# Kernel tuning notes

Hardware: AMD Instinct MI355X
Metric: run time of the kernel (lower is better)

## Reference

```python
import jax, jax.numpy as jnp
import numpy as np

D_MODEL = 1024
H = 16
D_K = D_MODEL // H
B = 128   # batch (intersample attention attends across this dim)
N = 256   # samples / tokens per row


def setup_inputs() -> dict:
    key = jax.random.key(0)
    ks = jax.random.split(key, 8)
    s = 1.0 / np.sqrt(D_MODEL)
    return {
        "query": jax.random.normal(ks[0], (B, N, D_MODEL), jnp.float32),
        "key":   jax.random.normal(ks[1], (B, N, D_MODEL), jnp.float32),
        "value": jax.random.normal(ks[2], (B, N, D_MODEL), jnp.float32),
        "Wq": jax.random.normal(ks[3], (D_MODEL, D_MODEL), jnp.float32) * s,
        "bq": jnp.zeros((D_MODEL,), jnp.float32),
        "Wk": jax.random.normal(ks[4], (D_MODEL, D_MODEL), jnp.float32) * s,
        "bk": jnp.zeros((D_MODEL,), jnp.float32),
        "Wv": jax.random.normal(ks[5], (D_MODEL, D_MODEL), jnp.float32) * s,
        "bv": jnp.zeros((D_MODEL,), jnp.float32),
        "Wo": jax.random.normal(ks[6], (D_MODEL, D_MODEL), jnp.float32) * s,
        "bo": jnp.zeros((D_MODEL,), jnp.float32),
    }


def _proj_heads(x, W, b):
    # torch nn.Linear: x @ W.T + b ; then view (b, n, h, d_k) -> (b, h, n, d_k)
    y = jnp.einsum('bnd,ed->bne', x, W) + b
    bsz, n, _ = y.shape
    return y.reshape(bsz, n, H, D_K).transpose(0, 2, 1, 3)


def reference(query, key, value, Wq, bq, Wk, bk, Wv, bv, Wo, bo):
    q = _proj_heads(query, Wq, bq)  # (b, h, n, d_k)
    k = _proj_heads(key,   Wk, bk)
    v = _proj_heads(value, Wv, bv)
    # intersample attention: attend ACROSS the batch dim b (per head, per sample n)
    scale = 1.0 / jnp.sqrt(jnp.asarray(D_K, q.dtype))
    scores = jnp.einsum('bhnd,chnd->hnbc', q, k) * scale  # (h, n, b, b)
    p = jax.nn.softmax(scores, axis=-1)
    out = jnp.einsum('hnbc,chnd->bhnd', p, v)             # (b, h, n, d_k)
    # merge heads: (b, h, n, d_k) -> (b, n, h*d_k)
    bsz, _, n, _ = out.shape
    out = out.transpose(0, 2, 1, 3).reshape(bsz, n, H * D_K)
    return jnp.einsum('bnd,ed->bne', out, Wo) + bo
```

## Files before the change

### kernel.cpp

```cpp
#include <hip/hip_runtime.h>
#include <hip/hip_bf16.h>
#include <stdint.h>

#define D_MODEL 1024
#define HEADS   16
#define DK      64
#define BATCH   128
#define NTOK    256
#define MROWS   (BATCH * NTOK)

typedef __attribute__((ext_vector_type(8))) short bf16x8;
typedef __attribute__((ext_vector_type(4))) float f32x4;

__device__ __forceinline__ unsigned short f2b_rne(float f) {
    union { float f; unsigned int u; } c; c.f = f;
    unsigned int u = c.u;
    unsigned int r = (u + 0x7FFFu + ((u >> 16) & 1u)) >> 16;
    return (unsigned short)r;
}

__device__ __forceinline__ void async16(const void* g, void* l) {
    __builtin_amdgcn_global_load_lds(
        (__attribute__((address_space(1))) void*)g,
        (__attribute__((address_space(3))) void*)l,
        16, 0, 0);
}

__global__ __launch_bounds__(256)
void f2b_kernel(const float* __restrict__ x, ushort* __restrict__ y, int n4) {
    int i = blockIdx.x * blockDim.x + threadIdx.x;
    int stride = gridDim.x * blockDim.x;
    for (; i < n4; i += stride) {
        float4 v = ((const float4*)x)[i];
        ushort4 o;
        o.x = f2b_rne(v.x); o.y = f2b_rne(v.y);
        o.z = f2b_rne(v.z); o.w = f2b_rne(v.w);
        ((ushort4*)y)[i] = o;
    }
}

__global__ __launch_bounds__(256)
void f2b2_kernel(const float* __restrict__ xa, const float* __restrict__ xc,
                 ushort* __restrict__ ya, ushort* __restrict__ yc, int n4) {
    int i = blockIdx.x * blockDim.x + threadIdx.x;
    int stride = gridDim.x * blockDim.x;
    for (; i < 2 * n4; i += stride) {
        const float* src = (i < n4) ? xa : xc;
        ushort*      dst = (i < n4) ? ya : yc;
        int j = (i < n4) ? i : i - n4;
        float4 v = ((const float4*)src)[j];
        ushort4 o;
        o.x = f2b_rne(v.x); o.y = f2b_rne(v.y);
        o.z = f2b_rne(v.z); o.w = f2b_rne(v.w);
        ((ushort4*)dst)[j] = o;
    }
}

__global__ __launch_bounds__(256)
void f2b4_kernel(const float* __restrict__ w0, const float* __restrict__ w1,
                 const float* __restrict__ w2, const float* __restrict__ w3,
                 ushort* __restrict__ y, int n4) {
    int i = blockIdx.x * blockDim.x + threadIdx.x;
    int stride = gridDim.x * blockDim.x;
    for (; i < 4 * n4; i += stride) {
        int sel = i / n4, j = i & (n4 - 1);
        const float* src = (sel == 0) ? w0 : (sel == 1) ? w1 : (sel == 2) ? w2 : w3;
        float4 v = ((const float4*)src)[j];
        ushort4 o;
        o.x = f2b_rne(v.x); o.y = f2b_rne(v.y);
        o.z = f2b_rne(v.z); o.w = f2b_rne(v.w);
        ((ushort4*)y)[i] = o;
    }
}

template<int MODE>
__global__ __launch_bounds__(512, 2)
void gemm_nt(const ushort* __restrict__ A, const ushort* __restrict__ B,
             const float* __restrict__ bias, void* __restrict__ Cout,
             int M, int N, int K, float alpha)
{
    __shared__ ushort smem[65536];

    const int tid  = threadIdx.x;
    const int wave = tid >> 6, lane = tid & 63;
    const int quad = lane >> 4, l15 = lane & 15;
    const int swz  = l15 & 7;

    const int o  = blockIdx.x;
    const int s  = (o & 7) * 64 + (o >> 3);
    const int pm = (s >> 2) * 256;
    const int pn = (s & 3) * 256;

    const int arow = (wave >> 2) * 128;
    const int brow = (wave & 3) * 64;

    const size_t laneoff = (size_t)(lane >> 3) * K
                         + (size_t)(((lane & 7) ^ (lane >> 3)) << 3);
    const ushort* Ab = A + (size_t)(pm + wave * 32) * K + laneoff;
    const ushort* Bb = B + (size_t)(pn + wave * 32) * K + laneoff;

    f32x4 acc[8][4] = {};
    bf16x8 afrag[4], bfrag[4];

#define STAGE(BUF, kt) do {                                                     \
    const ushort* ag_ = Ab + (size_t)(kt) * 64;                                 \
    const ushort* bg_ = Bb + (size_t)(kt) * 64;                                 \
    _Pragma("unroll")                                                           \
    for (int i_ = 0; i_ < 4; ++i_) {                                            \
        async16(ag_ + (size_t)(i_ * 8) * K,                                     \
                &smem[(BUF) * 32768 + wave * 2048 + i_ * 512]);                 \
        async16(bg_ + (size_t)(i_ * 8) * K,                                     \
                &smem[(BUF) * 32768 + 16384 + wave * 2048 + i_ * 512]);         \
    }                                                                           \
} while (0)

#define LDB(BUF, kkidx) do {                                                    \
    _Pragma("unroll")                                                           \
    for (int n_ = 0; n_ < 4; ++n_)                                              \
        bfrag[n_] = *(const bf16x8*)&smem[(BUF) * 32768 + 16384                 \
            + (brow + n_ * 16 + l15) * 64                                       \
            + ((((kkidx) * 4 + quad) ^ swz) << 3)];                             \
} while (0)

#define LDA(BUF, kkidx, qm) do {                                                \
    _Pragma("unroll")                                                           \
    for (int m_ = 0; m_ < 4; ++m_)                                              \
        afrag[m_] = *(const bf16x8*)&smem[(BUF) * 32768                         \
            + (arow + ((qm) * 4 + m_) * 16 + l15) * 64                          \
            + ((((kkidx) * 4 + quad) ^ swz) << 3)];                             \
} while (0)

#define MFMA16(qm) do {                                                         \
    __builtin_amdgcn_s_setprio(1);                                              \
    _Pragma("unroll")                                                           \
    for (int m_ = 0; m_ < 4; ++m_)                                              \
        _Pragma("unroll")                                                       \
        for (int n_ = 0; n_ < 4; ++n_)                                          \
            acc[(qm) * 4 + m_][n_] = __builtin_amdgcn_mfma_f32_16x16x32_bf16(   \
                afrag[m_], bfrag[n_], acc[(qm) * 4 + m_][n_], 0, 0, 0);         \
    __builtin_amdgcn_s_setprio(0);                                              \
} while (0)

#define PHASE_STD(BUF, kkidx, qm, RB) do {                                      \
    if (RB) LDB(BUF, kkidx);                                                    \
    LDA(BUF, kkidx, qm);                                                        \
    __builtin_amdgcn_s_barrier();                                               \
    asm volatile("s_waitcnt lgkmcnt(0)" ::: "memory");                          \
    __builtin_amdgcn_sched_barrier(0);                                          \
    MFMA16(qm);                                                                 \
    __builtin_amdgcn_s_barrier();                                               \
} while (0)

#define PHASE_LAST(BUF, kt, vmN) do {                                           \
    LDA(BUF, 1, 1);                                                             \
    asm volatile("s_waitcnt lgkmcnt(0)" ::: "memory");                          \
    __builtin_amdgcn_sched_barrier(0);                                          \
    __builtin_amdgcn_s_barrier();                                               \
    if ((kt) >= 0) STAGE(BUF, kt);                                              \
    MFMA16(1);                                                                  \
    if ((vmN) == 8)      { asm volatile("s_waitcnt vmcnt(8)" ::: "memory"); }   \
    else if ((vmN) == 0) { asm volatile("s_waitcnt vmcnt(0)" ::: "memory"); }   \
    __builtin_amdgcn_sched_barrier(0);                                          \
    __builtin_amdgcn_s_barrier();                                               \
} while (0)

    STAGE(0, 0);
    STAGE(1, 1);
    asm volatile("s_waitcnt vmcnt(8)" ::: "memory");
    __builtin_amdgcn_sched_barrier(0);
    __builtin_amdgcn_s_barrier();

    #pragma unroll 1
    for (int it = 0; it < 8; ++it) {
        const int t2 = 2 * it + 2;
        const int t3 = 2 * it + 3;
        PHASE_STD(0, 0, 0, 1);
        PHASE_STD(0, 0, 1, 0);
        PHASE_STD(0, 1, 0, 1);
        PHASE_LAST(0, (t2 < 16) ? t2 : -1, (t2 < 16) ? 8 : 0);
        PHASE_STD(1, 0, 0, 1);
        PHASE_STD(1, 0, 1, 0);
        PHASE_STD(1, 1, 0, 1);
        PHASE_LAST(1, (t3 < 16) ? t3 : -1, (t3 < 16) ? 8 : -1);
    }

#undef PHASE_LAST
#undef PHASE_STD
#undef MFMA16
#undef LDA
#undef LDB
#undef STAGE

    if (MODE == 0 || MODE == 2) {
        ushort* out = (ushort*)Cout;
        #pragma unroll
        for (int m = 0; m < 8; ++m) {
            const int mbase = pm + arow + m * 16 + quad * 4;
            #pragma unroll
            for (int n = 0; n < 4; ++n) {
                const int e = pn + brow + n * 16 + l15;
                const float bv = bias[e];
                const int h = e >> 6, d = e & 63;
                #pragma unroll
                for (int r = 0; r < 4; ++r) {
                    const int mm = mbase + r;
                    const int bb = mm >> 8, nn = mm & 255;
                    float val = (acc[m][n][r] + bv) * alpha;
                    size_t idx = (MODE == 0)
                        ? ((size_t)(((h << 8) + nn) * 128 + bb) * 64 + d)
                        : ((size_t)(((h << 8) + nn) * 64 + d) * 128 + bb);
                    out[idx] = f2b_rne(val);
                }
            }
        }
    } else {
        float* out = (float*)Cout;
        #pragma unroll
        for (int m = 0; m < 8; ++m) {
            const int mbase = pm + arow + m * 16 + quad * 4;
            #pragma unroll
            for (int n = 0; n < 4; ++n) {
                const int e = pn + brow + n * 16 + l15;
                const float bv = bias[e];
                #pragma unroll
                for (int r = 0; r < 4; ++r) {
                    const int mm = mbase + r;
                    out[(size_t)mm * N + e] = acc[m][n][r] + bv;
                }
            }
        }
    }
}

__global__ __launch_bounds__(256)
void attn_kernel(const ushort* __restrict__ Qp, const ushort* __restrict__ Kp,
                 const ushort* __restrict__ Vp, ushort* __restrict__ Ob)
{
    __shared__ __align__(16) ushort sm[24576];

    const int tid  = threadIdx.x;
    const int wave = tid >> 6, lane = tid & 63;
    const int quad = lane >> 4, l15 = lane & 15;
    const int sw   = l15 & 7;
    const int hn = blockIdx.x;
    const int h = hn >> 8, n = hn & 255;
    const size_t base = (size_t)hn * (BATCH * DK);

    {
        const uint4* Qg = (const uint4*)(Qp + base);
        const uint4* Kg = (const uint4*)(Kp + base);
        const uint4* Vg = (const uint4*)(Vp + base);
        uint4* s4 = (uint4*)sm;
        #pragma unroll
        for (int i = 0; i < 4; i++) {
            int id = tid + i * 256;
            int qr = id >> 3, qs = id & 7;
            int ql = qr * 8 + (qs ^ (qr & 7));
            s4[ql]        = Qg[id];
            s4[1024 + ql] = Kg[id];
            int vr = id >> 4, vs = id & 15;
            s4[2048 + vr * 16 + (vs ^ (vr & 7))] = Vg[id];
        }
    }
    __syncthreads();

    f32x4 accs[2][8] = {};
    #pragma unroll
    for (int kh = 0; kh < 2; kh++) {
        bf16x8 aq[2], bk8[8];
        #pragma unroll
        for (int mt = 0; mt < 2; mt++)
            aq[mt] = *(const bf16x8*)&sm[(wave * 32 + mt * 16 + l15) * 64
                                         + (((kh * 4 + quad) ^ sw) << 3)];
        #pragma unroll
        for (int nt = 0; nt < 8; nt++)
            bk8[nt] = *(const bf16x8*)&sm[8192 + (nt * 16 + l15) * 64
                                          + (((kh * 4 + quad) ^ sw) << 3)];
        __builtin_amdgcn_s_setprio(1);
        #pragma unroll
        for (int mt = 0; mt < 2; mt++)
            #pragma unroll
            for (int nt = 0; nt < 8; nt++)
                accs[mt][nt] = __builtin_amdgcn_mfma_f32_16x16x32_bf16(aq[mt], bk8[nt], accs[mt][nt], 0, 0, 0);
        __builtin_amdgcn_s_setprio(0);
    }

    #pragma unroll
    for (int mt = 0; mt < 2; mt++) {
        #pragma unroll
        for (int r = 0; r < 4; r++) {
            float mx = accs[mt][0][r];
            #pragma unroll
            for (int nt = 1; nt < 8; nt++) mx = fmaxf(mx, accs[mt][nt][r]);
            #pragma unroll
            for (int s = 1; s < 16; s <<= 1) mx = fmaxf(mx, __shfl_xor(mx, s, 64));
            float sum = 0.f;
            #pragma unroll
            for (int nt = 0; nt < 8; nt++) {
                float e = __expf(accs[mt][nt][r] - mx);
                accs[mt][nt][r] = e;
                sum += e;
            }
            #pragma unroll
            for (int s = 1; s < 16; s <<= 1) sum += __shfl_xor(sum, s, 64);
            float inv = 1.0f / sum;
            #pragma unroll
            for (int nt = 0; nt < 8; nt++) accs[mt][nt][r] *= inv;
        }
    }

    __syncthreads();

    #pragma unroll
    for (int mt = 0; mt < 2; mt++)
        #pragma unroll
        for (int nt = 0; nt < 8; nt++)
            #pragma unroll
            for (int r = 0; r < 4; r++) {
                int rw = wave * 32 + mt * 16 + quad * 4 + r;
                sm[rw * 128 + (((nt * 2 + (l15 >> 3)) ^ (rw & 7)) << 3) + (l15 & 7)] =
                    f2b_rne(accs[mt][nt][r]);
            }
    __syncthreads();

    f32x4 acco[2][4] = {};
    #pragma unroll
    for (int kh = 0; kh < 4; kh++) {
        bf16x8 ap[2], bv8[4];
        #pragma unroll
        for (int mt = 0; mt < 2; mt++)
            ap[mt] = *(const bf16x8*)&sm[(wave * 32 + mt * 16 + l15) * 128
                                         + (((kh * 4 + quad) ^ sw) << 3)];
        #pragma unroll
        for (int nt = 0; nt < 4; nt++)
            bv8[nt] = *(const bf16x8*)&sm[16384 + (nt * 16 + l15) * 128
                                          + (((kh * 4 + quad) ^ sw) << 3)];
        __builtin_amdgcn_s_setprio(1);
        #pragma unroll
        for (int mt = 0; mt < 2; mt++)
            #pragma unroll
            for (int nt = 0; nt < 4; nt++)
                acco[mt][nt] = __builtin_amdgcn_mfma_f32_16x16x32_bf16(ap[mt], bv8[nt], acco[mt][nt], 0, 0, 0);
        __builtin_amdgcn_s_setprio(0);
    }

    #pragma unroll
    for (int mt = 0; mt < 2; mt++)
        #pragma unroll
        for (int nt = 0; nt < 4; nt++)
            #pragma unroll
            for (int r = 0; r < 4; r++) {
                int b = wave * 32 + mt * 16 + quad * 4 + r;
                int d = nt * 16 + l15;
                Ob[((size_t)b * NTOK + n) * D_MODEL + h * DK + d] = f2b_rne(acco[mt][nt][r]);
            }
}

extern "C" void kernel_launch(void* const* d_in, const int* in_sizes, int n_in,
                              void* d_out, int out_size, void* d_ws, size_t ws_size,
                              hipStream_t stream)
{
    const float* q  = (const float*)d_in[0];
    const float* k  = (const float*)d_in[1];
    const float* v  = (const float*)d_in[2];
    const float* Wq = (const float*)d_in[3];
    const float* bq = (const float*)d_in[4];
    const float* Wk = (const float*)d_in[5];
    const float* bk = (const float*)d_in[6];
    const float* Wv = (const float*)d_in[7];
    const float* bv = (const float*)d_in[8];
    const float* Wo = (const float*)d_in[9];
    const float* bo = (const float*)d_in[10];

    const int XE = MROWS * D_MODEL;
    const int WE = D_MODEL * D_MODEL;

    ushort* xb = (ushort*)d_ws;
    ushort* Kp = xb + (size_t)XE;
    ushort* Vp = Kp + (size_t)XE;
    ushort* Wb = Vp + (size_t)XE;
    ushort* Qp = (ushort*)d_out;
    ushort* kb = Qp + (size_t)XE;

    dim3 blk(256);
    dim3 gblk(512);
    dim3 ggemm(512);

    f2b4_kernel<<<dim3(1024), blk, 0, stream>>>(Wq, Wk, Wv, Wo, Wb, WE / 4);

    f2b2_kernel<<<dim3(4096), blk, 0, stream>>>(q, k, xb, kb, XE / 4);

    gemm_nt<0><<<ggemm, gblk, 0, stream>>>(xb, Wb + 0 * (size_t)WE, bq, Qp,
                                           MROWS, D_MODEL, D_MODEL, 0.125f);
    gemm_nt<0><<<ggemm, gblk, 0, stream>>>(kb, Wb + 1 * (size_t)WE, bk, Kp,
                                           MROWS, D_MODEL, D_MODEL, 1.0f);
    f2b_kernel<<<dim3(4096), blk, 0, stream>>>(v, xb, XE / 4);
    gemm_nt<2><<<ggemm, gblk, 0, stream>>>(xb, Wb + 2 * (size_t)WE, bv, Vp,
                                           MROWS, D_MODEL, D_MODEL, 1.0f);

    attn_kernel<<<dim3(HEADS * NTOK), blk, 0, stream>>>(Qp, Kp, Vp, xb);

    gemm_nt<1><<<ggemm, gblk, 0, stream>>>(xb, Wb + 3 * (size_t)WE, bo, d_out,
                                           MROWS, D_MODEL, D_MODEL, 1.0f);
}
```

Measured before the change: 947.5 us.

## Store V row-major from projection and transpose into LDS inside attention kernel

The V projection GEMM now writes V in the same (h,n,b,d) layout as Q and K instead of a transposed (h,n,d,b) layout, avoiding scattered 2-byte global stores with a large stride in the GEMM epilogue. The attention kernel instead transposes V while loading it into shared memory, using per-element LDS writes. The LDS XOR swizzle for Q, K and P is also extended with higher row bits to reduce bank conflicts. The cost is more LDS store instructions, with possible bank conflicts, during the V staging in the attention kernel.

```diff
diff --git a/kernel.cpp b/kernel.cpp
--- a/kernel.cpp
+++ b/kernel.cpp
@@ -191,7 +191,7 @@
 #undef LDB
 #undef STAGE
 
-    if (MODE == 0 || MODE == 2) {
+    if (MODE == 0) {
         ushort* out = (ushort*)Cout;
         #pragma unroll
         for (int m = 0; m < 8; ++m) {
@@ -206,10 +206,7 @@
                     const int mm = mbase + r;
                     const int bb = mm >> 8, nn = mm & 255;
                     float val = (acc[m][n][r] + bv) * alpha;
-                    size_t idx = (MODE == 0)
-                        ? ((size_t)(((h << 8) + nn) * 128 + bb) * 64 + d)
-                        : ((size_t)(((h << 8) + nn) * 64 + d) * 128 + bb);
-                    out[idx] = f2b_rne(val);
+                    out[(size_t)(((h << 8) + nn) * 128 + bb) * 64 + d] = f2b_rne(val);
                 }
             }
         }
@@ -241,7 +238,6 @@
     const int tid  = threadIdx.x;
     const int wave = tid >> 6, lane = tid & 63;
     const int quad = lane >> 4, l15 = lane & 15;
-    const int sw   = l15 & 7;
     const int hn = blockIdx.x;
     const int h = hn >> 8, n = hn & 255;
     const size_t base = (size_t)hn * (BATCH * DK);
@@ -255,11 +251,17 @@
         for (int i = 0; i < 4; i++) {
             int id = tid + i * 256;
             int qr = id >> 3, qs = id & 7;
-            int ql = qr * 8 + (qs ^ (qr & 7));
+            int ql = qr * 8 + (qs ^ (qr & 7) ^ ((qr >> 3) & 7));
             s4[ql]        = Qg[id];
             s4[1024 + ql] = Kg[id];
-            int vr = id >> 4, vs = id & 15;
-            s4[2048 + vr * 16 + (vs ^ (vr & 7))] = Vg[id];
+            uint4 vv = Vg[id];
+            const ushort* vs = (const ushort*)&vv;
+            int b = id >> 3, i7 = id & 7;
+            #pragma unroll
+            for (int j = 0; j < 8; j++) {
+                int d = i7 * 8 + j;
+                sm[16384 + d * 128 + (((b >> 3) ^ j ^ i7) << 3) + (b & 7)] = vs[j];
+            }
         }
     }
     __syncthreads();
@@ -269,13 +271,17 @@
     for (int kh = 0; kh < 2; kh++) {
         bf16x8 aq[2], bk8[8];
         #pragma unroll
-        for (int mt = 0; mt < 2; mt++)
+        for (int mt = 0; mt < 2; mt++) {
+            int f = (l15 & 7) ^ ((wave * 4 + mt * 2 + (l15 >> 3)) & 7);
             aq[mt] = *(const bf16x8*)&sm[(wave * 32 + mt * 16 + l15) * 64
-                                         + (((kh * 4 + quad) ^ sw) << 3)];
-        #pragma unroll
-        for (int nt = 0; nt < 8; nt++)
+                                         + (((kh * 4 + quad) ^ f) << 3)];
+        }
+        #pragma unroll
+        for (int nt = 0; nt < 8; nt++) {
+            int f = (l15 & 7) ^ ((nt * 2 + (l15 >> 3)) & 7);
             bk8[nt] = *(const bf16x8*)&sm[8192 + (nt * 16 + l15) * 64
-                                          + (((kh * 4 + quad) ^ sw) << 3)];
+                                          + (((kh * 4 + quad) ^ f) << 3)];
+        }
         __builtin_amdgcn_s_setprio(1);
         #pragma unroll
         for (int mt = 0; mt < 2; mt++)
@@ -318,7 +324,8 @@
             #pragma unroll
             for (int r = 0; r < 4; r++) {
                 int rw = wave * 32 + mt * 16 + quad * 4 + r;
-                sm[rw * 128 + (((nt * 2 + (l15 >> 3)) ^ (rw & 7)) << 3) + (l15 & 7)] =
+                int f = ((quad * 4 + r) & 7) ^ ((wave * 4 + mt * 2 + (quad >> 1)) & 7);
+                sm[rw * 128 + (((nt * 2 + (l15 >> 3)) ^ f) << 3) + (l15 & 7)] =
                     f2b_rne(accs[mt][nt][r]);
             }
     __syncthreads();
@@ -328,13 +335,17 @@
     for (int kh = 0; kh < 4; kh++) {
         bf16x8 ap[2], bv8[4];
         #pragma unroll
-        for (int mt = 0; mt < 2; mt++)
+        for (int mt = 0; mt < 2; mt++) {
+            int f = (l15 & 7) ^ ((wave * 4 + mt * 2 + (l15 >> 3)) & 7);
             ap[mt] = *(const bf16x8*)&sm[(wave * 32 + mt * 16 + l15) * 128
-                                         + (((kh * 4 + quad) ^ sw) << 3)];
-        #pragma unroll
-        for (int nt = 0; nt < 4; nt++)
+                                         + (((kh * 4 + quad) ^ f) << 3)];
+        }
+        #pragma unroll
+        for (int nt = 0; nt < 4; nt++) {
+            int f = (l15 & 7) ^ ((nt * 2 + (l15 >> 3)) & 7);
             bv8[nt] = *(const bf16x8*)&sm[16384 + (nt * 16 + l15) * 128
-                                          + (((kh * 4 + quad) ^ sw) << 3)];
+                                          + (((kh * 4 + quad) ^ f) << 3)];
+        }
         __builtin_amdgcn_s_setprio(1);
         #pragma unroll
         for (int mt = 0; mt < 2; mt++)
@@ -395,7 +406,7 @@
     gemm_nt<0><<<ggemm, gblk, 0, stream>>>(kb, Wb + 1 * (size_t)WE, bk, Kp,
                                            MROWS, D_MODEL, D_MODEL, 1.0f);
     f2b_kernel<<<dim3(4096), blk, 0, stream>>>(v, xb, XE / 4);
-    gemm_nt<2><<<ggemm, gblk, 0, stream>>>(xb, Wb + 2 * (size_t)WE, bv, Vp,
+    gemm_nt<0><<<ggemm, gblk, 0, stream>>>(xb, Wb + 2 * (size_t)WE, bv, Vp,
                                            MROWS, D_MODEL, D_MODEL, 1.0f);
 
     attn_kernel<<<dim3(HEADS * NTOK), blk, 0, stream>>>(Qp, Kp, Vp, xb);
```

New measurement: 826.9 us. -12.7%, faster.
